# Optimization experiments

Measured on AMD Instinct MI355X. Metric: run time of the kernel, lower is better.

The kernel has to match this reference:

```python
import jax, jax.numpy as jnp
import numpy as np

TOPK = 9
NUM_CLASSES = 80
EPS = 1e-9


def _bbox_center(boxes):
    return jnp.stack([(boxes[..., 0] + boxes[..., 2]) * 0.5,
                      (boxes[..., 1] + boxes[..., 3]) * 0.5], axis=-1)


def _iou_batch(a, b):
    # a: [N, A, 4], b: [N, C, 4], xyxy -> [N, A, C]
    lt = jnp.maximum(a[:, :, None, :2], b[:, None, :, :2])
    rb = jnp.minimum(a[:, :, None, 2:], b[:, None, :, 2:])
    wh = jax.nn.relu(rb - lt)
    inter = wh[..., 0] * wh[..., 1]
    area_a = (a[..., 2] - a[..., 0]) * (a[..., 3] - a[..., 1])
    area_b = (b[..., 2] - b[..., 0]) * (b[..., 3] - b[..., 1])
    union = area_a[:, :, None] + area_b[:, None, :] - inter + 1e-9
    return inter / union


def _check_points_inside(points, bboxes, eps=EPS):
    # points [L,2], bboxes [B,n,4] -> [B,n,L] float (1 = center inside gt)
    x = points[None, None, :, 0]
    y = points[None, None, :, 1]
    xmin, ymin = bboxes[..., 0:1], bboxes[..., 1:2]
    xmax, ymax = bboxes[..., 2:3], bboxes[..., 3:4]
    dmin = jnp.minimum(jnp.minimum(x - xmin, y - ymin),
                       jnp.minimum(xmax - x, ymax - y))
    return (dmin > eps).astype(bboxes.dtype)


def _gather_topk_pyramid(dist, num_anchors_list, pad_gt_mask, topk):
    # dist: [B,n,L]; per pyramid level pick topk closest anchors per gt
    B, n, _ = dist.shape
    gt_mask = pad_gt_mask.astype(bool)  # [B,n,1]
    bi = jnp.arange(B)[:, None, None]
    gi = jnp.arange(n)[None, :, None]
    starts = [0] + list(np.cumsum(num_anchors_list)[:-1])
    is_in_topk_list, topk_idxs_list = [], []
    for na, start in zip(num_anchors_list, starts):
        d = jax.lax.dynamic_slice_in_dim(dist, start, na, axis=-1)
        _, topk_idxs = jax.lax.top_k(-d, topk)  # smallest distances -> [B,n,topk]
        topk_idxs_list.append(topk_idxs + start)
        idxs = jnp.where(gt_mask, topk_idxs, 0)
        # scatter-count (equivalent to one_hot(...).sum(-2)), then drop duplicates
        cnt = jnp.zeros((B, n, na), dist.dtype).at[bi, gi, idxs].add(1.0)
        is_in_topk_list.append(jnp.where(cnt > 1, 0.0, cnt))
    return jnp.concatenate(is_in_topk_list, -1), jnp.concatenate(topk_idxs_list, -1)


def reference(anchor_bboxes, num_anchors_list, gt_labels, gt_bboxes, pad_gt_mask, bg_index, pred_bboxes):
    L = anchor_bboxes.shape[0]
    B, n, _ = gt_bboxes.shape
    num_anchors_list = [int(v) for v in np.asarray(num_anchors_list)]
    # 1. iou between all gt and all anchors, [B,n,L]
    ious = _iou_batch(gt_bboxes.reshape(1, -1, 4), anchor_bboxes[None]).reshape(B, n, L)
    # 2. center distances, [B,n,L]
    gt_centers = _bbox_center(gt_bboxes)          # [B,n,2]
    anchor_centers = _bbox_center(anchor_bboxes)  # [L,2]
    diff = gt_centers[:, :, None, :] - anchor_centers[None, None, :, :]
    gt2anchor_distances = jnp.sqrt(jnp.sum(diff * diff, axis=-1))
    # 3. per-level topk closest candidates
    is_in_topk, topk_idxs = _gather_topk_pyramid(
        gt2anchor_distances, num_anchors_list, pad_gt_mask, TOPK)
    # 4. mean + std of candidate ious as threshold
    iou_candidates = ious * is_in_topk
    iou_threshold = jnp.take_along_axis(iou_candidates.reshape(B * n, L),
                                        topk_idxs.reshape(B * n, -1), axis=1)
    iou_threshold = iou_threshold.reshape(B, n, -1)
    iou_threshold = (jnp.mean(iou_threshold, axis=-1, keepdims=True)
                     + jnp.std(iou_threshold, axis=-1, keepdims=True, ddof=1))
    # 5. keep candidates above threshold
    is_in_topk = jnp.where(iou_candidates > iou_threshold, is_in_topk, 0.0)
    # 6. restrict centers to be inside gt
    is_in_gts = _check_points_inside(anchor_centers, gt_bboxes)
    mask_positive = is_in_topk * is_in_gts * pad_gt_mask  # [B,n,L]
    mask_positive_sum = mask_positive.sum(axis=-2)        # [B,L]
    # 7. anchors assigned to multiple gts -> keep highest-iou gt
    is_max_iou = (jnp.arange(n)[None, :, None] == ious.argmax(axis=-2)[:, None, :]).astype(ious.dtype)
    mask_positive = jnp.where(mask_positive_sum[:, None, :] > 1, is_max_iou, mask_positive)
    mask_positive_sum = mask_positive.sum(axis=-2)
    assigned_gt_index = mask_positive.argmax(axis=-2)     # [B,L]
    # gather assigned targets
    assigned_labels = jnp.take_along_axis(gt_labels[..., 0], assigned_gt_index, axis=1)
    assigned_labels = jnp.where(mask_positive_sum > 0, assigned_labels,
                                jnp.full_like(assigned_labels, bg_index))
    assigned_bboxes = jnp.take_along_axis(gt_bboxes, assigned_gt_index[..., None], axis=1)
    scores = jax.nn.one_hot(assigned_labels, NUM_CLASSES + 1, dtype=gt_bboxes.dtype)
    keep = np.array([i for i in range(NUM_CLASSES + 1) if i != bg_index])
    assigned_scores = scores[..., keep]                   # [B,L,C]
    # pred_bboxes given: scale scores by max positive iou per anchor
    pious = _iou_batch(gt_bboxes, pred_bboxes) * mask_positive
    assigned_scores = assigned_scores * pious.max(axis=-2)[..., None]
    return assigned_labels, assigned_bboxes, assigned_scores


def setup_inputs():
    key = jax.random.key(0)
    k1, k2, k3, k4 = jax.random.split(key, 4)
    B, n = 16, 64
    strides = [8, 16, 32, 64]
    anchors, num_anchors_list = [], []
    for s in strides:
        fs = 640 // s
        ys, xs = np.meshgrid(np.arange(fs), np.arange(fs), indexing='ij')
        cx = (xs + 0.5) * s
        cy = (ys + 0.5) * s
        half = 2.5 * s
        anchors.append(np.stack([cx - half, cy - half, cx + half, cy + half], -1).reshape(-1, 4))
        num_anchors_list.append(fs * fs)
    anchor_bboxes = jnp.asarray(np.concatenate(anchors, 0), jnp.float32)  # [8500,4]
    ctr = jax.random.uniform(k1, (B, n, 2), minval=32.0, maxval=608.0)
    wh = jax.random.uniform(k2, (B, n, 2), minval=16.0, maxval=256.0)
    gt_bboxes = jnp.concatenate([ctr - wh * 0.5, ctr + wh * 0.5], -1)
    gt_labels = jax.random.randint(k3, (B, n, 1), 0, NUM_CLASSES)
    pad_gt_mask = jnp.broadcast_to((jnp.arange(n) < 48).astype(jnp.float32)[None, :, None], (B, n, 1))
    pred_bboxes = anchor_bboxes[None] + 8.0 * jax.random.normal(k4, (B, anchor_bboxes.shape[0], 4))
    return {'anchor_bboxes': anchor_bboxes,
            'num_anchors_list': tuple(num_anchors_list),
            'gt_labels': gt_labels,
            'gt_bboxes': gt_bboxes,
            'pad_gt_mask': pad_gt_mask,
            'bg_index': NUM_CLASSES,
            'pred_bboxes': pred_bboxes}
```

## Files before the change

kernel.cpp:

```cpp
#include <hip/hip_runtime.h>

#define LC 8500
#define NC 64
#define BC 16
#define BLC (BC * LC)
#define NROWWAVES (BLC / 64)

typedef float f32x4v __attribute__((ext_vector_type(4)));

__device__ __forceinline__ float iou_box(float4 a, float4 b) {
    float ltx = fmaxf(a.x, b.x);
    float lty = fmaxf(a.y, b.y);
    float rbx = fminf(a.z, b.z);
    float rby = fminf(a.w, b.w);
    float w = fmaxf(rbx - ltx, 0.0f);
    float h = fmaxf(rby - lty, 0.0f);
    float inter = __fmul_rn(w, h);
    float area_a = __fmul_rn(a.z - a.x, a.w - a.y);
    float area_b = __fmul_rn(b.z - b.x, b.w - b.y);
    return inter / (area_a + area_b - inter + 1e-9f);
}

struct RoundRes { int won; float iou; int aidx; float4 ab; };

__device__ __forceinline__ RoundRes do_round(int lev_base, int lane,
                                             float gcx, float gcy, float4 g,
                                             const float4* __restrict__ anchors) {
    int active = (lane < 50) ? 1 : 0;
    int sub = (lane < 25) ? 0 : 1;
    int lev = lev_base + sub;
    int c = lane - sub * 25;
    int s = 8 << lev;
    int W = 80 >> lev;
    int start = (lev == 0) ? 0 : (lev == 1) ? 6400 : (lev == 2) ? 8000 : 8400;
    float inv_s = 1.0f / (float)s;
    int ixc = (int)(gcx * inv_s);
    int iyc = (int)(gcy * inv_s);
    int ix0 = min(max(ixc - 2, 0), W - 5);
    int iy0 = min(max(iyc - 2, 0), W - 5);
    int cm = c % 5, cd = c / 5;
    int cx = ix0 + cm;
    int cy = iy0 + cd;
    float acx = ((float)cx + 0.5f) * (float)s;
    float acy = ((float)cy + 0.5f) * (float)s;
    float dx = __fsub_rn(gcx, acx);
    float dy = __fsub_rn(gcy, acy);
    float d = sqrtf(__fadd_rn(__fmul_rn(dx, dx), __fmul_rn(dy, dy)));
    int aidx = start + cy * W + cx;
    unsigned long long key = active
        ? (((unsigned long long)__float_as_uint(d) << 32) | (unsigned)aidx)
        : ~0ull;
    int gbase = sub * 25;
    int rank = 0;
    #pragma unroll
    for (int delta = 1; delta < 25; ++delta) {
        int cs = c + delta;
        if (cs >= 25) cs -= 25;
        unsigned long long o = __shfl(key, gbase + cs);
        rank += (o < key) ? 1 : 0;
    }
    RoundRes r;
    r.won = active && (rank <= 8);
    r.aidx = aidx;
    r.iou = 0.0f;
    r.ab = make_float4(0.f, 0.f, 0.f, 0.f);
    if (r.won) {
        r.ab = anchors[aidx];
        r.iou = iou_box(g, r.ab);
    }
    return r;
}

__global__ __launch_bounds__(256) void topk_rank(
        const float4* __restrict__ anchors,
        const float4* __restrict__ gt,
        const float* __restrict__ pad_mask,
        unsigned* __restrict__ packed) {
    int bi = blockIdx.x * 4 + (threadIdx.x >> 6);
    int lane = threadIdx.x & 63;
    if (bi >= BC * NC) return;
    if (pad_mask[bi] == 0.0f) return;
    int b  = bi >> 6;
    int i  = bi & 63;

    float4 g = gt[bi];
    float gcx = (g.x + g.z) * 0.5f, gcy = (g.y + g.w) * 0.5f;

    RoundRes A = do_round(0, lane, gcx, gcy, g, anchors);
    RoundRes B = do_round(2, lane, gcx, gcy, g, anchors);

    float s = (A.won ? A.iou : 0.0f) + (B.won ? B.iou : 0.0f);
    #pragma unroll
    for (int off = 1; off < 64; off <<= 1) s += __shfl_xor(s, off);
    float mean = s / 36.0f;
    float da = A.won ? (A.iou - mean) : 0.0f;
    float db = B.won ? (B.iou - mean) : 0.0f;
    float ss = da * da + db * db;
    #pragma unroll
    for (int off = 1; off < 64; off <<= 1) ss += __shfl_xor(ss, off);
    float thr = mean + sqrtf(ss / 35.0f);

    unsigned claim = ((unsigned)i << 8) | 1u;
    size_t rowbase = (size_t)b * LC;
    if (A.won && A.iou > thr) {
        float acx = (A.ab.x + A.ab.z) * 0.5f, acy = (A.ab.y + A.ab.w) * 0.5f;
        float dmin = fminf(fminf(acx - g.x, acy - g.y), fminf(g.z - acx, g.w - acy));
        if (dmin > 1e-9f) atomicAdd(&packed[rowbase + (size_t)A.aidx], claim);
    }
    if (B.won && B.iou > thr) {
        float acx = (B.ab.x + B.ab.z) * 0.5f, acy = (B.ab.y + B.ab.w) * 0.5f;
        float dmin = fminf(fminf(acx - g.x, acy - g.y), fminf(g.z - acx, g.w - acy));
        if (dmin > 1e-9f) atomicAdd(&packed[rowbase + (size_t)B.aidx], claim);
    }
}

__global__ __launch_bounds__(256) void assign_scores_wave(
        const float4* __restrict__ anchors,
        const float4* __restrict__ gt,
        const int* __restrict__ gt_labels,
        const float4* __restrict__ pred,
        const unsigned* __restrict__ packed,
        const int* __restrict__ bg_index_p,
        float* __restrict__ out) {
    int wid  = (blockIdx.x * 256 + threadIdx.x) >> 6;
    int lane = threadIdx.x & 63;
    if (wid >= NROWWAVES) return;
    int t = wid * 64 + lane;
    int b = t / LC;
    int l = t - b * LC;

    unsigned pk = packed[t];
    unsigned c = pk & 0xFFu;
    int idx = 0;
    bool pos = false;
    if (c == 1u) {
        idx = (int)(pk >> 8);
        pos = true;
    } else if (c > 1u) {
        float4 abox = anchors[l];
        float best = -1.0f;
        int bi_ = 0;
        for (int ii = 0; ii < NC; ++ii) {
            float v = iou_box(gt[b * NC + ii], abox);
            if (v > best) { best = v; bi_ = ii; }
        }
        idx = bi_;
        pos = true;
    }
    int bg = *bg_index_p;
    int label = pos ? gt_labels[b * NC + idx] : bg;
    float4 gb = gt[b * NC + idx];
    float piou = pos ? iou_box(gb, pred[t]) : 0.0f;

    __builtin_nontemporal_store((float)label, out + t);
    f32x4v gv = { gb.x, gb.y, gb.z, gb.w };
    __builtin_nontemporal_store(gv, (f32x4v*)(out + BLC) + t);

    f32x4v* tile = (f32x4v*)(out + (size_t)BLC * 5) + (size_t)wid * 1280;
    #pragma unroll
    for (int k = 0; k < 20; ++k) {
        int f = k * 64 + lane;
        int rl = f / 20;
        int c0 = (f - rl * 20) * 4;
        int lr   = __shfl(label, rl);
        float pr = __shfl(piou,  rl);
        f32x4v v = { (c0 + 0 == lr) ? pr : 0.0f,
                     (c0 + 1 == lr) ? pr : 0.0f,
                     (c0 + 2 == lr) ? pr : 0.0f,
                     (c0 + 3 == lr) ? pr : 0.0f };
        __builtin_nontemporal_store(v, tile + f);
    }
}

extern "C" void kernel_launch(void* const* d_in, const int* in_sizes, int n_in,
                              void* d_out, int out_size, void* d_ws, size_t ws_size,
                              hipStream_t stream) {
    const float4* anchors    = (const float4*)d_in[0];
    const int*    gt_labels  = (const int*)d_in[2];
    const float4* gt         = (const float4*)d_in[3];
    const float*  pad_mask   = (const float*)d_in[4];
    const int*    bg_index_p = (const int*)d_in[5];
    const float4* pred       = (const float4*)d_in[6];

    unsigned* packed = (unsigned*)d_ws;
    float* out = (float*)d_out;

    hipMemsetAsync(packed, 0, (size_t)BLC * sizeof(unsigned), stream);
    hipLaunchKernelGGL(topk_rank, dim3((BC * NC) / 4), dim3(256), 0, stream,
                       anchors, gt, pad_mask, packed);
    hipLaunchKernelGGL(assign_scores_wave,
                       dim3((NROWWAVES * 64 + 255) / 256), dim3(256), 0, stream,
                       anchors, gt, gt_labels, pred, packed, bg_index_p, out);
}
```

Measured before the change: 31.56 us.

## Fuse top-k ranking and score assignment into one kernel with a global counter barrier

Merges the top-k ranking kernel and the per-anchor writer kernel into a single launch. The first 256 blocks do the ranking and atomic claims, then bump a global counter with release semantics. The remaining blocks spin on that counter with acquire loads before reading the packed claims. This removes one kernel launch and the inter-kernel gap, but needs all 788 blocks co-resident to avoid deadlock, and it adds a spin-wait.

```diff
diff --git a/kernel.cpp b/kernel.cpp
--- a/kernel.cpp
+++ b/kernel.cpp
@@ -5,6 +5,9 @@
 #define BC 16
 #define BLC (BC * LC)
 #define NROWWAVES (BLC / 64)
+#define TOPK_BLOCKS 256
+#define WRITER_BLOCKS 532
+#define TOTAL_BLOCKS (TOPK_BLOCKS + WRITER_BLOCKS)
 
 typedef float f32x4v __attribute__((ext_vector_type(4)));
 
@@ -71,65 +74,76 @@
     return r;
 }
 
-__global__ __launch_bounds__(256) void topk_rank(
-        const float4* __restrict__ anchors,
-        const float4* __restrict__ gt,
-        const float* __restrict__ pad_mask,
-        unsigned* __restrict__ packed) {
-    int bi = blockIdx.x * 4 + (threadIdx.x >> 6);
-    int lane = threadIdx.x & 63;
-    if (bi >= BC * NC) return;
-    if (pad_mask[bi] == 0.0f) return;
-    int b  = bi >> 6;
-    int i  = bi & 63;
-
-    float4 g = gt[bi];
-    float gcx = (g.x + g.z) * 0.5f, gcy = (g.y + g.w) * 0.5f;
-
-    RoundRes A = do_round(0, lane, gcx, gcy, g, anchors);
-    RoundRes B = do_round(2, lane, gcx, gcy, g, anchors);
-
-    float s = (A.won ? A.iou : 0.0f) + (B.won ? B.iou : 0.0f);
-    #pragma unroll
-    for (int off = 1; off < 64; off <<= 1) s += __shfl_xor(s, off);
-    float mean = s / 36.0f;
-    float da = A.won ? (A.iou - mean) : 0.0f;
-    float db = B.won ? (B.iou - mean) : 0.0f;
-    float ss = da * da + db * db;
-    #pragma unroll
-    for (int off = 1; off < 64; off <<= 1) ss += __shfl_xor(ss, off);
-    float thr = mean + sqrtf(ss / 35.0f);
-
-    unsigned claim = ((unsigned)i << 8) | 1u;
-    size_t rowbase = (size_t)b * LC;
-    if (A.won && A.iou > thr) {
-        float acx = (A.ab.x + A.ab.z) * 0.5f, acy = (A.ab.y + A.ab.w) * 0.5f;
-        float dmin = fminf(fminf(acx - g.x, acy - g.y), fminf(g.z - acx, g.w - acy));
-        if (dmin > 1e-9f) atomicAdd(&packed[rowbase + (size_t)A.aidx], claim);
-    }
-    if (B.won && B.iou > thr) {
-        float acx = (B.ab.x + B.ab.z) * 0.5f, acy = (B.ab.y + B.ab.w) * 0.5f;
-        float dmin = fminf(fminf(acx - g.x, acy - g.y), fminf(g.z - acx, g.w - acy));
-        if (dmin > 1e-9f) atomicAdd(&packed[rowbase + (size_t)B.aidx], claim);
-    }
-}
-
-__global__ __launch_bounds__(256) void assign_scores_wave(
+__global__ __launch_bounds__(256, 4) void fused_assign(
         const float4* __restrict__ anchors,
         const float4* __restrict__ gt,
         const int* __restrict__ gt_labels,
         const float4* __restrict__ pred,
-        const unsigned* __restrict__ packed,
+        const float* __restrict__ pad_mask,
         const int* __restrict__ bg_index_p,
+        unsigned* __restrict__ packed,
+        unsigned* __restrict__ counter,
         float* __restrict__ out) {
-    int wid  = (blockIdx.x * 256 + threadIdx.x) >> 6;
     int lane = threadIdx.x & 63;
+
+    if (blockIdx.x < TOPK_BLOCKS) {
+        int bi = blockIdx.x * 4 + (threadIdx.x >> 6);
+        if (pad_mask[bi] != 0.0f) {
+            int b = bi >> 6;
+            int i = bi & 63;
+            float4 g = gt[bi];
+            float gcx = (g.x + g.z) * 0.5f, gcy = (g.y + g.w) * 0.5f;
+
+            RoundRes A = do_round(0, lane, gcx, gcy, g, anchors);
+            RoundRes B = do_round(2, lane, gcx, gcy, g, anchors);
+
+            float s = (A.won ? A.iou : 0.0f) + (B.won ? B.iou : 0.0f);
+            #pragma unroll
+            for (int off = 1; off < 64; off <<= 1) s += __shfl_xor(s, off);
+            float mean = s / 36.0f;
+            float da = A.won ? (A.iou - mean) : 0.0f;
+            float db = B.won ? (B.iou - mean) : 0.0f;
+            float ss = da * da + db * db;
+            #pragma unroll
+            for (int off = 1; off < 64; off <<= 1) ss += __shfl_xor(ss, off);
+            float thr = mean + sqrtf(ss / 35.0f);
+
+            unsigned claim = ((unsigned)i << 8) | 1u;
+            size_t rowbase = (size_t)b * LC;
+            if (A.won && A.iou > thr) {
+                float acx = (A.ab.x + A.ab.z) * 0.5f, acy = (A.ab.y + A.ab.w) * 0.5f;
+                float dmin = fminf(fminf(acx - g.x, acy - g.y), fminf(g.z - acx, g.w - acy));
+                if (dmin > 1e-9f) atomicAdd(&packed[rowbase + (size_t)A.aidx], claim);
+            }
+            if (B.won && B.iou > thr) {
+                float acx = (B.ab.x + B.ab.z) * 0.5f, acy = (B.ab.y + B.ab.w) * 0.5f;
+                float dmin = fminf(fminf(acx - g.x, acy - g.y), fminf(g.z - acx, g.w - acy));
+                if (dmin > 1e-9f) atomicAdd(&packed[rowbase + (size_t)B.aidx], claim);
+            }
+        }
+        __threadfence();
+        __syncthreads();
+        if (threadIdx.x == 0)
+            __hip_atomic_fetch_add(counter, 1u, __ATOMIC_RELEASE,
+                                   __HIP_MEMORY_SCOPE_AGENT);
+        return;
+    }
+
+    if (threadIdx.x == 0) {
+        while (__hip_atomic_load(counter, __ATOMIC_ACQUIRE,
+                                 __HIP_MEMORY_SCOPE_AGENT) < TOPK_BLOCKS)
+            __builtin_amdgcn_s_sleep(2);
+    }
+    __syncthreads();
+
+    int wid = (blockIdx.x - TOPK_BLOCKS) * 4 + (threadIdx.x >> 6);
     if (wid >= NROWWAVES) return;
     int t = wid * 64 + lane;
     int b = t / LC;
     int l = t - b * LC;
 
-    unsigned pk = packed[t];
+    unsigned pk = __hip_atomic_load(&packed[t], __ATOMIC_RELAXED,
+                                    __HIP_MEMORY_SCOPE_AGENT);
     unsigned c = pk & 0xFFu;
     int idx = 0;
     bool pos = false;
@@ -182,13 +196,12 @@
     const int*    bg_index_p = (const int*)d_in[5];
     const float4* pred       = (const float4*)d_in[6];
 
-    unsigned* packed = (unsigned*)d_ws;
+    unsigned* packed  = (unsigned*)d_ws;
+    unsigned* counter = packed + BLC;
     float* out = (float*)d_out;
 
-    hipMemsetAsync(packed, 0, (size_t)BLC * sizeof(unsigned), stream);
-    hipLaunchKernelGGL(topk_rank, dim3((BC * NC) / 4), dim3(256), 0, stream,
-                       anchors, gt, pad_mask, packed);
-    hipLaunchKernelGGL(assign_scores_wave,
-                       dim3((NROWWAVES * 64 + 255) / 256), dim3(256), 0, stream,
-                       anchors, gt, gt_labels, pred, packed, bg_index_p, out);
-}
+    hipMemsetAsync(packed, 0, ((size_t)BLC + 1) * sizeof(unsigned), stream);
+    hipLaunchKernelGGL(fused_assign, dim3(TOTAL_BLOCKS), dim3(256), 0, stream,
+                       anchors, gt, gt_labels, pred, pad_mask, bg_index_p,
+                       packed, counter, out);
+}
```

Measured after the change: 86.02 us. 2.73x slower.
